# Performance work log

Measured on AMD Instinct MI355X. Metric: run time of the kernel, lower is better.

Reference implementation:

```python
import jax, jax.numpy as jnp
import numpy as np

B, KL, XL, DIM, H, PB = 4, 128, 4096, 256, 8, 8
HD = DIM // H
SCALE = HD ** -0.5
N_DIS = 64 + 2


def setup_inputs() -> dict:
    key = jax.random.key(0)
    ks = jax.random.split(key, 10)
    x = jax.random.normal(ks[0], (B, XL, DIM), jnp.float32)
    kernal = jax.random.normal(ks[1], (B, KL, DIM), jnp.float32)
    rd = jax.random.randint(ks[2], (B, KL, XL), 0, N_DIS)
    polar_pos = jax.random.randint(ks[3], (B, KL, XL), 0, PB)
    att_mask = jax.random.uniform(ks[4], (B, H, XL, KL)) < 0.1
    W_qkv = jax.random.normal(ks[5], (DIM, 3 * DIM), jnp.float32) * 0.02
    dis_embed = jax.random.normal(ks[6], (N_DIS, H), jnp.float32) * 0.02
    polar_emb = jax.random.normal(ks[7], (PB, 1), jnp.float32) * 0.02
    W_proj = jax.random.normal(ks[8], (DIM, DIM), jnp.float32) * 0.02
    b_proj = jnp.zeros((DIM,), jnp.float32)
    return dict(x=x, kernal=kernal, rd=rd, polar_pos=polar_pos, att_mask=att_mask,
                W_qkv=W_qkv, dis_embed=dis_embed, polar_emb=polar_emb,
                W_proj=W_proj, b_proj=b_proj)


def _heads(t, h):
    b, n, d = t.shape
    return t.reshape(b, n, h, d // h).transpose(0, 2, 1, 3)  # b h n hd


def reference(x, kernal, rd, polar_pos, att_mask, W_qkv, dis_embed, polar_emb, W_proj, b_proj):
    b, xl, dim = x.shape
    kl = kernal.shape[1]
    h = H
    scale = (dim // h) ** -0.5

    q, k, v = [_heads(t, h) for t in jnp.split(x @ W_qkv, 3, axis=-1)]        # b h xl hd
    k_q, k_k, k_v = [_heads(t, h) for t in jnp.split(kernal @ W_qkv, 3, axis=-1)]  # b h kl hd

    rd_e = dis_embed[rd].transpose(0, 3, 1, 2)  # (b,kl,xl,h) -> (b,h,kl,xl)

    # kernel -> x attention scores
    k_x_attn = jnp.einsum('bhkd,bhxd->bhkx', k_q, k) * scale  # b h kl xl

    # main orientation: one-hot-weighted |attn| reduced over x, argmax over polar bins
    pp = jnp.broadcast_to(polar_pos[:, None], (b, h, kl, xl))  # b h kl xl
    polar_hot = jax.nn.one_hot(pp, PB, dtype=k_x_attn.dtype)   # b h kl xl o
    ori_sum = jnp.einsum('bhkx,bhkxo->bhko', jnp.abs(k_x_attn), polar_hot)
    main_ori = jnp.argmax(ori_sum, axis=-1)                    # b h kl
    new_polar = pp - main_ori[..., None]
    new_polar = jnp.where(new_polar < 0, new_polar + PB, new_polar)
    polar_bias = polar_emb[new_polar, 0]                       # b h kl xl

    mask_k = att_mask.transpose(0, 1, 3, 2)                    # b h kl xl
    k_x_attn = jnp.where(mask_k, jnp.asarray(-1e6, k_x_attn.dtype), k_x_attn)
    attn_k = jax.nn.softmax(k_x_attn + rd_e + polar_bias, axis=-1)
    k_out = jnp.einsum('bhkx,bhxd->bhkd', attn_k, v)
    k_out = k_out.transpose(0, 2, 1, 3).reshape(b, kl, dim) @ W_proj + b_proj

    # x -> kernel attention scores
    x_k_attn = jnp.einsum('bhxd,bhkd->bhxk', q, k_k) * scale   # b h xl kl
    x_k_attn = jnp.where(att_mask, jnp.asarray(-1e9, x_k_attn.dtype), x_k_attn)
    x_k_attn = jax.nn.softmax(x_k_attn + rd_e.transpose(0, 1, 3, 2)
                              + polar_bias.transpose(0, 1, 3, 2), axis=-1)
    x_out = jnp.einsum('bhxk,bhkd->bhxd', x_k_attn, k_v)
    x_out = x_out.transpose(0, 2, 1, 3).reshape(b, xl, dim) @ W_proj + b_proj

    return (x_out, k_out)
```

## Files before the change

kernel.cpp:

```cpp
#include <hip/hip_runtime.h>
#include <hip/hip_bf16.h>

#define B_    4
#define KL_   128
#define XL_   4096
#define DIM_  256
#define H_    8
#define HD_   32
#define PB_   8
#define NDIS_ 66
#define TDIM_ 768
#define SCALE_ 0.17677669529663687f
#define NS_   4
#define XCH_  (XL_ / NS_)
#define NCH2_ 64
#define KC2_  16

typedef float v4f __attribute__((ext_vector_type(4)));
typedef short v8s __attribute__((ext_vector_type(8)));

__device__ __forceinline__ unsigned short f2bf(float f) {
    __hip_bfloat16 h = __float2bfloat16(f);
    return __builtin_bit_cast(unsigned short, h);
}
__device__ __forceinline__ float bf2f(unsigned short u) {
    return __bfloat162float(__builtin_bit_cast(__hip_bfloat16, u));
}
__device__ __forceinline__ void cvt_hilo(float v, unsigned short& hi, unsigned short& lo) {
    hi = f2bf(v);
    lo = f2bf(v - bf2f(hi));
}

__global__ __launch_bounds__(256) void cvt_mat(const float* __restrict__ A,
                                               unsigned short* __restrict__ Ah,
                                               unsigned short* __restrict__ Al,
                                               size_t n4) {
    size_t i = ((size_t)blockIdx.x * 256 + threadIdx.x);
    if (i >= n4) return;
    float4 v = *(const float4*)&A[i * 4];
    ushort4 h, l;
    cvt_hilo(v.x, h.x, l.x);
    cvt_hilo(v.y, h.y, l.y);
    cvt_hilo(v.z, h.z, l.z);
    cvt_hilo(v.w, h.w, l.w);
    *(ushort4*)&Ah[i * 4] = h;
    *(ushort4*)&Al[i * 4] = l;
}

__global__ __launch_bounds__(256) void cvt_wT(const float* __restrict__ W,
                                              unsigned short* __restrict__ Wh,
                                              unsigned short* __restrict__ Wl,
                                              int K, int N) {
    int n = blockIdx.x, k = threadIdx.x;
    float v = W[(size_t)k * N + n];
    unsigned short h, l;
    cvt_hilo(v, h, l);
    Wh[(size_t)n * K + k] = h;
    Wl[(size_t)n * K + k] = l;
}

__global__ __launch_bounds__(256) void cvt_kq(const float* __restrict__ qkv_k,
                                              unsigned short* __restrict__ Kqh_g,
                                              unsigned short* __restrict__ Kql_g) {
    const int bh = blockIdx.x;
    const int b = bh >> 3, h = bh & 7;
    const int tid = threadIdx.x;
    const int k = tid >> 1, dg = (tid & 1) * 16;
    const float* src = &qkv_k[((size_t)(b * KL_ + k)) * TDIM_ + h * HD_ + dg];
    unsigned short hi[16], lo[16];
#pragma unroll
    for (int j4 = 0; j4 < 4; ++j4) {
        float4 v = *(const float4*)&src[j4 * 4];
        cvt_hilo(v.x, hi[j4 * 4 + 0], lo[j4 * 4 + 0]);
        cvt_hilo(v.y, hi[j4 * 4 + 1], lo[j4 * 4 + 1]);
        cvt_hilo(v.z, hi[j4 * 4 + 2], lo[j4 * 4 + 2]);
        cvt_hilo(v.w, hi[j4 * 4 + 3], lo[j4 * 4 + 3]);
    }
    unsigned short* dh = &Kqh_g[((size_t)bh * KL_ + k) * HD_ + dg];
    unsigned short* dl = &Kql_g[((size_t)bh * KL_ + k) * HD_ + dg];
    *(uint4*)&dh[0] = *(uint4*)&hi[0];
    *(uint4*)&dh[8] = *(uint4*)&hi[8];
    *(uint4*)&dl[0] = *(uint4*)&lo[0];
    *(uint4*)&dl[8] = *(uint4*)&lo[8];
}

__global__ __launch_bounds__(256) void gemm_mfma(const unsigned short* __restrict__ Ah,
                                                 const unsigned short* __restrict__ Al,
                                                 const unsigned short* __restrict__ Bh,
                                                 const unsigned short* __restrict__ Bl,
                                                 float* __restrict__ C,
                                                 const float* __restrict__ bias,
                                                 int M, int N, int K) {
    __shared__ __align__(16) unsigned short Ah_s[128][40];
    __shared__ __align__(16) unsigned short Al_s[128][40];
    __shared__ __align__(16) unsigned short Bh_s[128][40];
    __shared__ __align__(16) unsigned short Bl_s[128][40];
    const int tid = threadIdx.x;
    const int w = tid >> 6, lane = tid & 63;
    const int c = lane & 15, q = lane >> 4;
    const int bm = blockIdx.y * 128, bn = blockIdx.x * 128;
    const int srow = tid >> 1, shf = (tid & 1) * 16;

    v4f acc[2][8] = {};
    for (int k0 = 0; k0 < K; k0 += 32) {
        __syncthreads();
        {
            const size_t ab = (size_t)(bm + srow) * K + k0 + shf;
            *(uint4*)&Ah_s[srow][shf] = *(const uint4*)&Ah[ab];
            *(uint4*)&Ah_s[srow][shf + 8] = *(const uint4*)&Ah[ab + 8];
            *(uint4*)&Al_s[srow][shf] = *(const uint4*)&Al[ab];
            *(uint4*)&Al_s[srow][shf + 8] = *(const uint4*)&Al[ab + 8];
            const size_t bb = (size_t)(bn + srow) * K + k0 + shf;
            *(uint4*)&Bh_s[srow][shf] = *(const uint4*)&Bh[bb];
            *(uint4*)&Bh_s[srow][shf + 8] = *(const uint4*)&Bh[bb + 8];
            *(uint4*)&Bl_s[srow][shf] = *(const uint4*)&Bl[bb];
            *(uint4*)&Bl_s[srow][shf + 8] = *(const uint4*)&Bl[bb + 8];
        }
        __syncthreads();
        v8s afh[2], afl[2];
#pragma unroll
        for (int mt = 0; mt < 2; ++mt) {
            afh[mt] = *(v8s*)&Ah_s[w * 32 + mt * 16 + c][q * 8];
            afl[mt] = *(v8s*)&Al_s[w * 32 + mt * 16 + c][q * 8];
        }
#pragma unroll
        for (int nt = 0; nt < 8; ++nt) {
            v8s bfh = *(v8s*)&Bh_s[nt * 16 + c][q * 8];
            v8s bfl = *(v8s*)&Bl_s[nt * 16 + c][q * 8];
#pragma unroll
            for (int mt = 0; mt < 2; ++mt) {
                acc[mt][nt] = __builtin_amdgcn_mfma_f32_16x16x32_bf16(afl[mt], bfh, acc[mt][nt], 0, 0, 0);
                acc[mt][nt] = __builtin_amdgcn_mfma_f32_16x16x32_bf16(afh[mt], bfl, acc[mt][nt], 0, 0, 0);
                acc[mt][nt] = __builtin_amdgcn_mfma_f32_16x16x32_bf16(afh[mt], bfh, acc[mt][nt], 0, 0, 0);
            }
        }
    }
#pragma unroll
    for (int mt = 0; mt < 2; ++mt) {
#pragma unroll
        for (int nt = 0; nt < 8; ++nt) {
            int col = bn + nt * 16 + c;
            float bv = bias ? bias[col] : 0.0f;
#pragma unroll
            for (int r = 0; r < 4; ++r) {
                int row = bm + w * 32 + mt * 16 + q * 4 + r;
                C[(size_t)row * N + col] = acc[mt][nt][r] + bv;
            }
        }
    }
}

__global__ __launch_bounds__(256) void gemm64(const float* __restrict__ A,
                                              const float* __restrict__ Bw,
                                              float* __restrict__ C,
                                              const float* __restrict__ bias,
                                              int M, int N, int K) {
    __shared__ __align__(16) float As[16][68];
    __shared__ __align__(16) float Bs[16][64];
    const int tid = threadIdx.x;
    const int tx = tid & 15, ty = tid >> 4;
    const int bn = blockIdx.x * 64, bm = blockIdx.y * 64;
    const int am = tid >> 2, ac = tid & 3;
    float acc[4][4] = {};
    for (int k0 = 0; k0 < K; k0 += 16) {
        float4 a4 = *(const float4*)&A[(size_t)(bm + am) * K + k0 + ac * 4];
        As[ac * 4 + 0][am] = a4.x;
        As[ac * 4 + 1][am] = a4.y;
        As[ac * 4 + 2][am] = a4.z;
        As[ac * 4 + 3][am] = a4.w;
        *(float4*)&Bs[ty][tx * 4] = *(const float4*)&Bw[(size_t)(k0 + ty) * N + bn + tx * 4];
        __syncthreads();
#pragma unroll
        for (int kk = 0; kk < 16; ++kk) {
            float4 av = *(const float4*)&As[kk][ty * 4];
            float4 bv = *(const float4*)&Bs[kk][tx * 4];
            float a[4] = {av.x, av.y, av.z, av.w};
            float b[4] = {bv.x, bv.y, bv.z, bv.w};
#pragma unroll
            for (int i = 0; i < 4; ++i)
#pragma unroll
                for (int j = 0; j < 4; ++j) acc[i][j] += a[i] * b[j];
        }
        __syncthreads();
    }
#pragma unroll
    for (int i = 0; i < 4; ++i) {
        int m = bm + ty * 4 + i;
#pragma unroll
        for (int j = 0; j < 4; ++j) {
            int n = bn + tx * 4 + j;
            float v = acc[i][j];
            if (bias) v += bias[n];
            C[(size_t)m * N + n] = v;
        }
    }
}

__global__ __launch_bounds__(256) void score_bins_mfma4(const float* __restrict__ qkv_x,
                                                        const unsigned short* __restrict__ Kqh_g,
                                                        const unsigned short* __restrict__ Kql_g,
                                                        const int* __restrict__ rd,
                                                        const int* __restrict__ polar_pos,
                                                        const int* __restrict__ att_mask,
                                                        const float* __restrict__ dis_embed,
                                                        __hip_bfloat16* __restrict__ Sg,
                                                        float* __restrict__ binspart) {
    const int b = blockIdx.z, h = blockIdx.y, xc = blockIdx.x;
    const int x0 = xc * 64;
    const int tid = threadIdx.x;
    const int w = tid >> 6, lane = tid & 63;
    const int c15 = lane & 15, q = lane >> 4;
    const size_t bh = (size_t)(b * H_ + h);

    __shared__ unsigned int mskb[64][5];
    __shared__ float de_h[NDIS_];
    __shared__ float binsL[8][4][16][PB_];

    {
        int xr = tid >> 2, kg = tid & 3;
        size_t gb = (bh * XL_ + x0 + xr) * KL_ + kg * 32;
        unsigned bits = 0;
#pragma unroll
        for (int i = 0; i < 8; ++i) {
            int4 m4 = *(const int4*)&att_mask[gb + i * 4];
            bits |= (m4.x ? 1u : 0u) << (i * 4 + 0);
            bits |= (m4.y ? 1u : 0u) << (i * 4 + 1);
            bits |= (m4.z ? 1u : 0u) << (i * 4 + 2);
            bits |= (m4.w ? 1u : 0u) << (i * 4 + 3);
        }
        mskb[xr][kg] = bits;
    }
    if (tid < NDIS_) de_h[tid] = dis_embed[tid * H_ + h];
    __syncthreads();

    v8s axh, axl;
    {
        const float* src = &qkv_x[((size_t)b * XL_ + x0 + w * 16 + c15) * TDIM_ + DIM_ + h * HD_ + q * 8];
        float4 v0 = *(const float4*)&src[0];
        float4 v1 = *(const float4*)&src[4];
        float vv[8] = {v0.x, v0.y, v0.z, v0.w, v1.x, v1.y, v1.z, v1.w};
#pragma unroll
        for (int j = 0; j < 8; ++j) {
            unsigned short hi, lo;
            cvt_hilo(vv[j], hi, lo);
            ((short*)&axh)[j] = (short)hi;
            ((short*)&axl)[j] = (short)lo;
        }
    }

    v8s bqh[2], bql[2];
    int4 r4[2], p4[2];
    auto load_nt = [&](int nt, int s) {
        const int k = nt * 16 + c15;
        const size_t kqoff = (bh * KL_ + k) * HD_ + q * 8;
        bqh[s] = *(const v8s*)&Kqh_g[kqoff];
        bql[s] = *(const v8s*)&Kql_g[kqoff];
        const size_t rowoff = ((size_t)(b * KL_ + k)) * XL_ + x0 + w * 16 + q * 4;
        r4[s] = *(const int4*)&rd[rowoff];
        p4[s] = *(const int4*)&polar_pos[rowoff];
    };
    load_nt(0, 0);

#pragma unroll
    for (int nt = 0; nt < 8; ++nt) {
        const int s = nt & 1;
        if (nt < 7) load_nt(nt + 1, s ^ 1);

        const int k = nt * 16 + c15;
        v4f D = {0.f, 0.f, 0.f, 0.f};
        D = __builtin_amdgcn_mfma_f32_16x16x32_bf16(axl, bqh[s], D, 0, 0, 0);
        D = __builtin_amdgcn_mfma_f32_16x16x32_bf16(axh, bql[s], D, 0, 0, 0);
        D = __builtin_amdgcn_mfma_f32_16x16x32_bf16(axh, bqh[s], D, 0, 0, 0);

        float bins[PB_] = {};
        {
            int rv[4] = {r4[s].x, r4[s].y, r4[s].z, r4[s].w};
            int pv[4] = {p4[s].x, p4[s].y, p4[s].z, p4[s].w};
            ushort4 pack;
#pragma unroll
            for (int r = 0; r < 4; ++r) {
                float sc = D[r] * SCALE_;
                float a = fabsf(sc);
                int pp = pv[r];
#pragma unroll
                for (int pb = 0; pb < PB_; ++pb) bins[pb] += (pp == pb) ? a : 0.0f;
                int xloc = w * 16 + q * 4 + r;
                int mbit = (mskb[xloc][k >> 5] >> (k & 31)) & 1;
                float sp = (mbit ? -1e6f : sc) + de_h[rv[r]];
                ((unsigned short*)&pack)[r] = f2bf(sp);
            }
            *(ushort4*)((unsigned short*)Sg + (bh * KL_ + k) * XL_ + x0 + w * 16 + q * 4) = pack;
        }

#pragma unroll
        for (int pb = 0; pb < PB_; ++pb) {
            bins[pb] += __shfl_xor(bins[pb], 16);
            bins[pb] += __shfl_xor(bins[pb], 32);
        }
        if (q == 0) {
#pragma unroll
            for (int pb = 0; pb < PB_; ++pb) binsL[nt][w][c15][pb] = bins[pb];
        }
    }
    __syncthreads();
    {
        int k = tid >> 1, half = tid & 1;
        int nt = k >> 4, c = k & 15;
        float4 s = {0.f, 0.f, 0.f, 0.f};
#pragma unroll
        for (int w4 = 0; w4 < 4; ++w4) {
            float4 v = *(float4*)&binsL[nt][w4][c][half * 4];
            s.x += v.x; s.y += v.y; s.z += v.z; s.w += v.w;
        }
        *(float4*)&binspart[(bh * KL_ + k) * (NCH2_ * PB_) + xc * PB_ + half * 4] = s;
    }
}

__global__ __launch_bounds__(256) void bins_argmax(const float* __restrict__ binspart,
                                                   int* __restrict__ main_ori) {
    const int w = threadIdx.x >> 6, lane = threadIdx.x & 63;
    const int row = blockIdx.x * 4 + w;
    float s[PB_];
#pragma unroll
    for (int pb = 0; pb < PB_; ++pb) s[pb] = 0.0f;
    if (lane < NCH2_) {
        const float* bp = &binspart[(size_t)row * (NCH2_ * PB_) + lane * PB_];
#pragma unroll
        for (int pb = 0; pb < PB_; ++pb) s[pb] = bp[pb];
    }
#pragma unroll
    for (int m = 1; m < 64; m <<= 1)
#pragma unroll
        for (int pb = 0; pb < PB_; ++pb) s[pb] += __shfl_xor(s[pb], m);
    if (lane == 0) {
        float best = s[0];
        int bi = 0;
#pragma unroll
        for (int pb = 1; pb < PB_; ++pb)
            if (s[pb] > best) { best = s[pb]; bi = pb; }
        main_ori[row] = bi;
    }
}

__global__ __launch_bounds__(256) void flash_cached2(const float* __restrict__ qkv_x,
                                                     const __hip_bfloat16* __restrict__ Sg,
                                                     const int* __restrict__ polar_pos,
                                                     const float* __restrict__ polar_emb,
                                                     const int* __restrict__ main_ori,
                                                     float* __restrict__ part) {
    const int b = blockIdx.z, h = blockIdx.y;
    const int kch = blockIdx.x / NS_, xc = blockIdx.x % NS_;
    const int k0 = kch * KC2_;
    const int tid = threadIdx.x;
    const int ki = tid >> 4, xt = tid & 15;

    __shared__ __align__(16) float4 vs[64][9];
    __shared__ int pol_s[KC2_][68];
    __shared__ float pe[PB_];

    if (tid < PB_) pe[tid] = polar_emb[tid];
    const size_t xbase = (size_t)b * XL_;
    const size_t bh = (size_t)(b * H_ + h);
    const size_t row_k = bh * KL_ + k0 + ki;
    const int mo = main_ori[row_k];
    const int xbeg = xc * XCH_;

    float l = 0.f;
    float4 acc[8] = {};
    __syncthreads();
    for (int t = 0; t < XCH_ / 64; ++t) {
        const int x0 = xbeg + t * 64;
        __syncthreads();
#pragma unroll
        for (int i = 0; i < 2; ++i) {
            int id = tid + 256 * i;
            int row = id >> 3, c = id & 7;
            vs[row][c] = *(const float4*)&qkv_x[(xbase + x0 + row) * TDIM_ + 2 * DIM_ + h * HD_ + c * 4];
        }
        {
            int kk = tid >> 4, c = tid & 15;
            *(int4*)&pol_s[kk][c * 4] =
                *(const int4*)&polar_pos[(size_t)(b * KL_ + k0 + kk) * XL_ + x0 + c * 4];
        }
        __syncthreads();
#pragma unroll
        for (int j = 0; j < 4; ++j) {
            int xl = xt + 16 * j;
            int x = x0 + xl;
            float sp = __bfloat162float(Sg[row_k * XL_ + x]);
            int pp = pol_s[ki][xl];
            int np = pp - mo;
            np += (np >> 31) & PB_;
            float p = __expf(sp + pe[np]);
            l += p;
#pragma unroll
            for (int c = 0; c < 8; ++c) {
                float4 v = vs[xl][c];
                acc[c].x += p * v.x; acc[c].y += p * v.y;
                acc[c].z += p * v.z; acc[c].w += p * v.w;
            }
        }
    }
#pragma unroll
    for (int m = 1; m < 16; m <<= 1) {
        l += __shfl_xor(l, m, 16);
#pragma unroll
        for (int c = 0; c < 8; ++c) {
            acc[c].x += __shfl_xor(acc[c].x, m, 16);
            acc[c].y += __shfl_xor(acc[c].y, m, 16);
            acc[c].z += __shfl_xor(acc[c].z, m, 16);
            acc[c].w += __shfl_xor(acc[c].w, m, 16);
        }
    }
    if (xt == 0) {
        float* dst = &part[(size_t)(row_k * NS_ + xc) * 36];
#pragma unroll
        for (int c = 0; c < 8; ++c) *(float4*)&dst[c * 4] = acc[c];
        dst[32] = l;
    }
}

__global__ __launch_bounds__(256) void merge_cached(const float* __restrict__ part,
                                                    float* __restrict__ kout_pre) {
    const int tid = threadIdx.x;
    const int ri = tid >> 5, d = tid & 31;
    const int row = blockIdx.x * 8 + ri;
    float l = 0.f, a = 0.f;
#pragma unroll
    for (int c = 0; c < NS_; ++c) {
        const float* p = &part[(size_t)(row * NS_ + c) * 36];
        l += p[32];
        a += p[d];
    }
    int k = row & (KL_ - 1);
    int bh = row >> 7;
    int h = bh & (H_ - 1), b = bh >> 3;
    kout_pre[(size_t)(b * KL_ + k) * DIM_ + h * HD_ + d] = a / l;
}

__global__ __launch_bounds__(256) void attn_x_mfma(const float* __restrict__ qkv_x,
                                                   const float* __restrict__ qkv_k,
                                                   const int* __restrict__ rd,
                                                   const int* __restrict__ polar_pos,
                                                   const int* __restrict__ att_mask,
                                                   const float* __restrict__ dis_embed,
                                                   const float* __restrict__ polar_emb,
                                                   const int* __restrict__ main_ori,
                                                   unsigned short* __restrict__ oh,
                                                   unsigned short* __restrict__ ol) {
    const int b = blockIdx.z, h = blockIdx.y;
    const int x0 = blockIdx.x * 64;
    const int tid = threadIdx.x;
    const int wave = tid >> 6, lane = tid & 63;
    const int c = lane & 15, q = lane >> 4;

    __shared__ __align__(16) unsigned short Kk_s[KL_][40];
    __shared__ __align__(16) unsigned short VT_s[HD_][136];
    __shared__ __align__(16) unsigned short P_s[4][16][136];
    __shared__ unsigned short rp_s[KL_][72];
    __shared__ float de_h[NDIS_];
    __shared__ float pe[PB_];
    __shared__ int mo_s[KL_];

    const size_t bh = (size_t)(b * H_ + h);
    if (tid < NDIS_) de_h[tid] = dis_embed[tid * H_ + h];
    if (tid < PB_) pe[tid] = polar_emb[tid];
    if (tid < KL_) mo_s[tid] = main_ori[bh * KL_ + tid];

    {
        int row = tid >> 1, half = tid & 1;
        const float* src = &qkv_k[(size_t)(b * KL_ + row) * TDIM_ + h * HD_ + half * 16];
#pragma unroll
        for (int j = 0; j < 16; ++j) Kk_s[row][half * 16 + j] = f2bf(src[DIM_ + j]);
#pragma unroll
        for (int j = 0; j < 16; ++j) VT_s[half * 16 + j][row] = f2bf(src[2 * DIM_ + j]);
    }
    __syncthreads();

#pragma unroll
    for (int i = 0; i < 8; ++i) {
        int id = tid + 256 * i;
        int k = id >> 4, cc = id & 15;
        size_t gb = (size_t)(b * KL_ + k) * XL_ + x0 + cc * 4;
        int4 r4 = *(const int4*)&rd[gb];
        int4 p4 = *(const int4*)&polar_pos[gb];
        int mo = mo_s[k];
        int n0 = p4.x - mo; n0 += (n0 >> 31) & PB_;
        int n1 = p4.y - mo; n1 += (n1 >> 31) & PB_;
        int n2 = p4.z - mo; n2 += (n2 >> 31) & PB_;
        int n3 = p4.w - mo; n3 += (n3 >> 31) & PB_;
        rp_s[k][cc * 4 + 0] = (unsigned short)(r4.x | (n0 << 8));
        rp_s[k][cc * 4 + 1] = (unsigned short)(r4.y | (n1 << 8));
        rp_s[k][cc * 4 + 2] = (unsigned short)(r4.z | (n2 << 8));
        rp_s[k][cc * 4 + 3] = (unsigned short)(r4.w | (n3 << 8));
    }
    __syncthreads();
#pragma unroll
    for (int i = 0; i < 8; ++i) {
        int id = tid + 256 * i;
        int xr = id >> 5, kc = id & 31;
        int4 m4 = *(const int4*)&att_mask[(bh * XL_ + x0 + xr) * KL_ + kc * 4];
        if (m4.x) rp_s[kc * 4 + 0][xr] |= 0x8000;
        if (m4.y) rp_s[kc * 4 + 1][xr] |= 0x8000;
        if (m4.z) rp_s[kc * 4 + 2][xr] |= 0x8000;
        if (m4.w) rp_s[kc * 4 + 3][xr] |= 0x8000;
    }
    __syncthreads();

    v8s aq;
    {
        const float* qp = &qkv_x[(size_t)(b * XL_ + x0 + wave * 16 + c) * TDIM_ + h * HD_ + q * 8];
        float4 q0 = *(const float4*)&qp[0];
        float4 q1 = *(const float4*)&qp[4];
        aq[0] = (short)f2bf(q0.x); aq[1] = (short)f2bf(q0.y);
        aq[2] = (short)f2bf(q0.z); aq[3] = (short)f2bf(q0.w);
        aq[4] = (short)f2bf(q1.x); aq[5] = (short)f2bf(q1.y);
        aq[6] = (short)f2bf(q1.z); aq[7] = (short)f2bf(q1.w);
    }

    v4f S[8];
#pragma unroll
    for (int t = 0; t < 8; ++t) {
        v8s bk = *(v8s*)&Kk_s[t * 16 + c][q * 8];
        S[t] = __builtin_amdgcn_mfma_f32_16x16x32_bf16(aq, bk, (v4f){0.f, 0.f, 0.f, 0.f}, 0, 0, 0);
    }

    const int xloc = wave * 16;
    float lr[4] = {0.f, 0.f, 0.f, 0.f};
#pragma unroll
    for (int t = 0; t < 8; ++t) {
#pragma unroll
        for (int r = 0; r < 4; ++r) {
            int krow = t * 16 + c;
            int xrow = q * 4 + r;
            unsigned short rp = rp_s[krow][xloc + xrow];
            float sval = S[t][r] * SCALE_;
            float tval = ((rp & 0x8000) ? -25.0f : sval) + de_h[rp & 0x7f] + pe[(rp >> 8) & 7];
            float p = __expf(tval);
            unsigned short pb = f2bf(p);
            P_s[wave][xrow][krow] = pb;
            lr[r] += bf2f(pb);
        }
    }
#pragma unroll
    for (int r = 0; r < 4; ++r) {
#pragma unroll
        for (int m = 1; m < 16; m <<= 1) lr[r] += __shfl_xor(lr[r], m);
    }
    __syncthreads();

    v4f O0 = {0.f, 0.f, 0.f, 0.f}, O1 = {0.f, 0.f, 0.f, 0.f};
#pragma unroll
    for (int kc = 0; kc < 4; ++kc) {
        v8s ap = *(v8s*)&P_s[wave][c][kc * 32 + q * 8];
        v8s bv0 = *(v8s*)&VT_s[c][kc * 32 + q * 8];
        v8s bv1 = *(v8s*)&VT_s[16 + c][kc * 32 + q * 8];
        O0 = __builtin_amdgcn_mfma_f32_16x16x32_bf16(ap, bv0, O0, 0, 0, 0);
        O1 = __builtin_amdgcn_mfma_f32_16x16x32_bf16(ap, bv1, O1, 0, 0, 0);
    }

#pragma unroll
    for (int r = 0; r < 4; ++r) {
        int xg = x0 + wave * 16 + q * 4 + r;
        float inv = 1.0f / lr[r];
        size_t obase = (size_t)(b * XL_ + xg) * DIM_ + h * HD_;
        float v0 = O0[r] * inv;
        float v1 = O1[r] * inv;
        unsigned short h0, l0, h1, l1;
        cvt_hilo(v0, h0, l0);
        cvt_hilo(v1, h1, l1);
        oh[obase + c] = h0;
        ol[obase + c] = l0;
        oh[obase + 16 + c] = h1;
        ol[obase + 16 + c] = l1;
    }
}

extern "C" void kernel_launch(void* const* d_in, const int* in_sizes, int n_in,
                              void* d_out, int out_size, void* d_ws, size_t ws_size,
                              hipStream_t stream) {
    const float* x         = (const float*)d_in[0];
    const float* kernal    = (const float*)d_in[1];
    const int* rd          = (const int*)d_in[2];
    const int* polar_pos   = (const int*)d_in[3];
    const int* att_mask    = (const int*)d_in[4];
    const float* W_qkv     = (const float*)d_in[5];
    const float* dis_embed = (const float*)d_in[6];
    const float* polar_emb = (const float*)d_in[7];
    const float* W_proj    = (const float*)d_in[8];
    const float* b_proj    = (const float*)d_in[9];
    float* out             = (float*)d_out;

    char* base = (char*)d_ws;
    size_t off = 0;
    auto alloc = [&](size_t bytes) { void* p = base + off; off = (off + bytes + 255) & ~255ULL; return p; };
    float* qkv_x    = (float*)alloc((size_t)B_ * XL_ * TDIM_ * 4);
    float* qkv_k    = (float*)alloc((size_t)B_ * KL_ * TDIM_ * 4);
    float* xout_pre = (float*)alloc((size_t)B_ * XL_ * DIM_ * 4);
    float* kout_pre = (float*)alloc((size_t)B_ * KL_ * DIM_ * 4);
    int* main_ori   = (int*)alloc(B_ * H_ * KL_ * 4);
    float* part     = (float*)alloc((size_t)B_ * H_ * KL_ * NS_ * 36 * 4);
    __hip_bfloat16* Sg = (__hip_bfloat16*)alloc((size_t)B_ * H_ * KL_ * XL_ * 2);
    unsigned short* wph = (unsigned short*)alloc((size_t)DIM_ * DIM_ * 2);
    unsigned short* wpl = (unsigned short*)alloc((size_t)DIM_ * DIM_ * 2);

    float* binspart = xout_pre;
    const size_t MX = (size_t)B_ * XL_;
    unsigned short* xh = (unsigned short*)Sg;
    unsigned short* xl_ = xh + MX * DIM_;
    unsigned short* wqh = (unsigned short*)part;
    unsigned short* wql = wqh + (size_t)TDIM_ * DIM_;
    unsigned short* kqh_g = wqh + 2 * (size_t)TDIM_ * DIM_;
    unsigned short* kql_g = kqh_g + (size_t)B_ * H_ * KL_ * HD_;
    unsigned short* oh = (unsigned short*)Sg;
    unsigned short* ol = oh + MX * DIM_;

    cvt_mat<<<dim3((MX * DIM_ / 4 + 255) / 256), 256, 0, stream>>>(x, xh, xl_, MX * DIM_ / 4);
    cvt_wT<<<dim3(TDIM_), DIM_, 0, stream>>>(W_qkv, wqh, wql, DIM_, TDIM_);
    cvt_wT<<<dim3(DIM_), DIM_, 0, stream>>>(W_proj, wph, wpl, DIM_, DIM_);

    gemm_mfma<<<dim3(TDIM_ / 128, MX / 128), 256, 0, stream>>>(
        xh, xl_, wqh, wql, qkv_x, nullptr, MX, TDIM_, DIM_);
    gemm64<<<dim3(TDIM_ / 64, (B_ * KL_) / 64), 256, 0, stream>>>(
        kernal, W_qkv, qkv_k, nullptr, B_ * KL_, TDIM_, DIM_);
    cvt_kq<<<dim3(B_ * H_), 256, 0, stream>>>(qkv_k, kqh_g, kql_g);

    score_bins_mfma4<<<dim3(NCH2_, H_, B_), 256, 0, stream>>>(
        qkv_x, kqh_g, kql_g, rd, polar_pos, att_mask, dis_embed, Sg, binspart);
    bins_argmax<<<dim3(B_ * H_ * KL_ / 4), 256, 0, stream>>>(binspart, main_ori);
    flash_cached2<<<dim3((KL_ / KC2_) * NS_, H_, B_), 256, 0, stream>>>(
        qkv_x, Sg, polar_pos, polar_emb, main_ori, part);
    merge_cached<<<dim3(B_ * H_ * KL_ / 8), 256, 0, stream>>>(part, kout_pre);

    attn_x_mfma<<<dim3(XL_ / 64, H_, B_), 256, 0, stream>>>(
        qkv_x, qkv_k, rd, polar_pos, att_mask, dis_embed, polar_emb, main_ori, oh, ol);

    gemm_mfma<<<dim3(DIM_ / 128, MX / 128), 256, 0, stream>>>(
        oh, ol, wph, wpl, out, b_proj, MX, DIM_, DIM_);
    gemm64<<<dim3(DIM_ / 64, (B_ * KL_) / 64), 256, 0, stream>>>(
        kout_pre, W_proj, out + (size_t)B_ * XL_ * DIM_, b_proj, B_ * KL_, DIM_, DIM_);
}
```

Before: 362.0 us.

## Prepack attention mask into bitfield once and use LDS atomics for bins

Adds a pack_mask kernel that converts the int32 attention mask into 32-bit bitmasks once. Both score_bins_mfma4 and attn_x_mfma then read the compact bits instead of each scanning the full int mask, which is meant to cut redundant global traffic. Separately, the per-polar-bin reductions in score_bins are replaced by shared-memory atomicAdd into a [KL][PB+1] array, removing the shuffle reductions and staging buffer. The cost is an extra kernel launch plus LDS atomic contention, since all 16 x positions of a k row hit the same bins.

New measurement: 402.3 us. 1.11x slower.

```diff
diff --git a/kernel.cpp b/kernel.cpp
--- a/kernel.cpp
+++ b/kernel.cpp
@@ -29,6 +29,22 @@
 __device__ __forceinline__ void cvt_hilo(float v, unsigned short& hi, unsigned short& lo) {
     hi = f2bf(v);
     lo = f2bf(v - bf2f(hi));
+}
+
+__global__ __launch_bounds__(256) void pack_mask(const int* __restrict__ att_mask,
+                                                 unsigned int* __restrict__ mbits) {
+    size_t wid = (size_t)blockIdx.x * 256 + threadIdx.x;
+    const int* src = &att_mask[wid * 32];
+    unsigned bits = 0;
+#pragma unroll
+    for (int i = 0; i < 8; ++i) {
+        int4 m4 = *(const int4*)&src[i * 4];
+        bits |= (m4.x ? 1u : 0u) << (i * 4 + 0);
+        bits |= (m4.y ? 1u : 0u) << (i * 4 + 1);
+        bits |= (m4.z ? 1u : 0u) << (i * 4 + 2);
+        bits |= (m4.w ? 1u : 0u) << (i * 4 + 3);
+    }
+    mbits[wid] = bits;
 }
 
 __global__ __launch_bounds__(256) void cvt_mat(const float* __restrict__ A,
@@ -201,7 +217,7 @@
                                                         const unsigned short* __restrict__ Kql_g,
                                                         const int* __restrict__ rd,
                                                         const int* __restrict__ polar_pos,
-                                                        const int* __restrict__ att_mask,
+                                                        const unsigned int* __restrict__ mbits,
                                                         const float* __restrict__ dis_embed,
                                                         __hip_bfloat16* __restrict__ Sg,
                                                         float* __restrict__ binspart) {
@@ -214,23 +230,14 @@
 
     __shared__ unsigned int mskb[64][5];
     __shared__ float de_h[NDIS_];
-    __shared__ float binsL[8][4][16][PB_];
+    __shared__ float bins_s[KL_][PB_ + 1];
 
     {
         int xr = tid >> 2, kg = tid & 3;
-        size_t gb = (bh * XL_ + x0 + xr) * KL_ + kg * 32;
-        unsigned bits = 0;
-#pragma unroll
-        for (int i = 0; i < 8; ++i) {
-            int4 m4 = *(const int4*)&att_mask[gb + i * 4];
-            bits |= (m4.x ? 1u : 0u) << (i * 4 + 0);
-            bits |= (m4.y ? 1u : 0u) << (i * 4 + 1);
-            bits |= (m4.z ? 1u : 0u) << (i * 4 + 2);
-            bits |= (m4.w ? 1u : 0u) << (i * 4 + 3);
-        }
-        mskb[xr][kg] = bits;
+        mskb[xr][kg] = mbits[(bh * XL_ + x0 + xr) * 4 + kg];
     }
     if (tid < NDIS_) de_h[tid] = dis_embed[tid * H_ + h];
+    for (int i = tid; i < KL_ * (PB_ + 1); i += 256) ((float*)bins_s)[i] = 0.0f;
     __syncthreads();
 
     v8s axh, axl;
@@ -272,7 +279,6 @@
         D = __builtin_amdgcn_mfma_f32_16x16x32_bf16(axh, bql[s], D, 0, 0, 0);
         D = __builtin_amdgcn_mfma_f32_16x16x32_bf16(axh, bqh[s], D, 0, 0, 0);
 
-        float bins[PB_] = {};
         {
             int rv[4] = {r4[s].x, r4[s].y, r4[s].z, r4[s].w};
             int pv[4] = {p4[s].x, p4[s].y, p4[s].z, p4[s].w};
@@ -281,9 +287,7 @@
             for (int r = 0; r < 4; ++r) {
                 float sc = D[r] * SCALE_;
                 float a = fabsf(sc);
-                int pp = pv[r];
-#pragma unroll
-                for (int pb = 0; pb < PB_; ++pb) bins[pb] += (pp == pb) ? a : 0.0f;
+                atomicAdd(&bins_s[k][pv[r]], a);
                 int xloc = w * 16 + q * 4 + r;
                 int mbit = (mskb[xloc][k >> 5] >> (k & 31)) & 1;
                 float sp = (mbit ? -1e6f : sc) + de_h[rv[r]];
@@ -291,27 +295,15 @@
             }
             *(ushort4*)((unsigned short*)Sg + (bh * KL_ + k) * XL_ + x0 + w * 16 + q * 4) = pack;
         }
-
-#pragma unroll
-        for (int pb = 0; pb < PB_; ++pb) {
-            bins[pb] += __shfl_xor(bins[pb], 16);
-            bins[pb] += __shfl_xor(bins[pb], 32);
-        }
-        if (q == 0) {
-#pragma unroll
-            for (int pb = 0; pb < PB_; ++pb) binsL[nt][w][c15][pb] = bins[pb];
-        }
     }
     __syncthreads();
     {
         int k = tid >> 1, half = tid & 1;
-        int nt = k >> 4, c = k & 15;
-        float4 s = {0.f, 0.f, 0.f, 0.f};
-#pragma unroll
-        for (int w4 = 0; w4 < 4; ++w4) {
-            float4 v = *(float4*)&binsL[nt][w4][c][half * 4];
-            s.x += v.x; s.y += v.y; s.z += v.z; s.w += v.w;
-        }
+        float4 s;
+        s.x = bins_s[k][half * 4 + 0];
+        s.y = bins_s[k][half * 4 + 1];
+        s.z = bins_s[k][half * 4 + 2];
+        s.w = bins_s[k][half * 4 + 3];
         *(float4*)&binspart[(bh * KL_ + k) * (NCH2_ * PB_) + xc * PB_ + half * 4] = s;
     }
 }
@@ -442,7 +434,7 @@
                                                    const float* __restrict__ qkv_k,
                                                    const int* __restrict__ rd,
                                                    const int* __restrict__ polar_pos,
-                                                   const int* __restrict__ att_mask,
+                                                   const unsigned int* __restrict__ mbits,
                                                    const float* __restrict__ dis_embed,
                                                    const float* __restrict__ polar_emb,
                                                    const int* __restrict__ main_ori,
@@ -458,6 +450,7 @@
     __shared__ __align__(16) unsigned short VT_s[HD_][136];
     __shared__ __align__(16) unsigned short P_s[4][16][136];
     __shared__ unsigned short rp_s[KL_][72];
+    __shared__ unsigned int msk_s[64][5];
     __shared__ float de_h[NDIS_];
     __shared__ float pe[PB_];
     __shared__ int mo_s[KL_];
@@ -474,6 +467,10 @@
         for (int j = 0; j < 16; ++j) Kk_s[row][half * 16 + j] = f2bf(src[DIM_ + j]);
 #pragma unroll
         for (int j = 0; j < 16; ++j) VT_s[half * 16 + j][row] = f2bf(src[2 * DIM_ + j]);
+    }
+    {
+        int xr = tid >> 2, kg = tid & 3;
+        msk_s[xr][kg] = mbits[(bh * XL_ + x0 + xr) * 4 + kg];
     }
     __syncthreads();
 
@@ -495,17 +492,6 @@
         rp_s[k][cc * 4 + 3] = (unsigned short)(r4.w | (n3 << 8));
     }
     __syncthreads();
-#pragma unroll
-    for (int i = 0; i < 8; ++i) {
-        int id = tid + 256 * i;
-        int xr = id >> 5, kc = id & 31;
-        int4 m4 = *(const int4*)&att_mask[(bh * XL_ + x0 + xr) * KL_ + kc * 4];
-        if (m4.x) rp_s[kc * 4 + 0][xr] |= 0x8000;
-        if (m4.y) rp_s[kc * 4 + 1][xr] |= 0x8000;
-        if (m4.z) rp_s[kc * 4 + 2][xr] |= 0x8000;
-        if (m4.w) rp_s[kc * 4 + 3][xr] |= 0x8000;
-    }
-    __syncthreads();
 
     v8s aq;
     {
@@ -534,8 +520,9 @@
             int krow = t * 16 + c;
             int xrow = q * 4 + r;
             unsigned short rp = rp_s[krow][xloc + xrow];
+            int mbit = (msk_s[xloc + xrow][krow >> 5] >> (krow & 31)) & 1;
             float sval = S[t][r] * SCALE_;
-            float tval = ((rp & 0x8000) ? -25.0f : sval) + de_h[rp & 0x7f] + pe[(rp >> 8) & 7];
+            float tval = (mbit ? -25.0f : sval) + de_h[rp & 0x7f] + pe[(rp >> 8) & 7];
             float p = __expf(tval);
             unsigned short pb = f2bf(p);
             P_s[wave][xrow][krow] = pb;
@@ -603,6 +590,7 @@
     __hip_bfloat16* Sg = (__hip_bfloat16*)alloc((size_t)B_ * H_ * KL_ * XL_ * 2);
     unsigned short* wph = (unsigned short*)alloc((size_t)DIM_ * DIM_ * 2);
     unsigned short* wpl = (unsigned short*)alloc((size_t)DIM_ * DIM_ * 2);
+    unsigned int* mbits = (unsigned int*)alloc((size_t)B_ * H_ * XL_ * (KL_ / 32) * 4);
 
     float* binspart = xout_pre;
     const size_t MX = (size_t)B_ * XL_;
@@ -615,6 +603,7 @@
     unsigned short* oh = (unsigned short*)Sg;
     unsigned short* ol = oh + MX * DIM_;
 
+    pack_mask<<<dim3((B_ * H_ * XL_ * (KL_ / 32)) / 256), 256, 0, stream>>>(att_mask, mbits);
     cvt_mat<<<dim3((MX * DIM_ / 4 + 255) / 256), 256, 0, stream>>>(x, xh, xl_, MX * DIM_ / 4);
     cvt_wT<<<dim3(TDIM_), DIM_, 0, stream>>>(W_qkv, wqh, wql, DIM_, TDIM_);
     cvt_wT<<<dim3(DIM_), DIM_, 0, stream>>>(W_proj, wph, wpl, DIM_, DIM_);
@@ -626,14 +615,14 @@
     cvt_kq<<<dim3(B_ * H_), 256, 0, stream>>>(qkv_k, kqh_g, kql_g);
 
     score_bins_mfma4<<<dim3(NCH2_, H_, B_), 256, 0, stream>>>(
-        qkv_x, kqh_g, kql_g, rd, polar_pos, att_mask, dis_embed, Sg, binspart);
+        qkv_x, kqh_g, kql_g, rd, polar_pos, mbits, dis_embed, Sg, binspart);
     bins_argmax<<<dim3(B_ * H_ * KL_ / 4), 256, 0, stream>>>(binspart, main_ori);
     flash_cached2<<<dim3((KL_ / KC2_) * NS_, H_, B_), 256, 0, stream>>>(
         qkv_x, Sg, polar_pos, polar_emb, main_ori, part);
     merge_cached<<<dim3(B_ * H_ * KL_ / 8), 256, 0, stream>>>(part, kout_pre);
 
     attn_x_mfma<<<dim3(XL_ / 64, H_, B_), 256, 0, stream>>>(
-        qkv_x, qkv_k, rd, polar_pos, att_mask, dis_embed, polar_emb, main_ori, oh, ol);
+        qkv_x, qkv_k, rd, polar_pos, mbits, dis_embed, polar_emb, main_ori, oh, ol);
 
     gemm_mfma<<<dim3(DIM_ / 128, MX / 128), 256, 0, stream>>>(
         oh, ol, wph, wpl, out, b_proj, MX, DIM_, DIM_);
```
